# Performance work log

Measured on AMD Instinct MI355X. Metric: run time of the kernel, lower is better.

The kernel has to match this reference:

```python
import jax, jax.numpy as jnp
import numpy as np

LN_EPS = 1e-5


def setup_inputs() -> dict:
    key = jax.random.key(0)
    ks = jax.random.split(key, 6)
    N, E, D = 100000, 600000, 128
    x = jax.random.normal(ks[0], (N, D), dtype=jnp.float32)
    edge_index = jax.random.randint(ks[1], (2, E), 0, N, dtype=jnp.int64)
    dropout_mask = jax.random.uniform(ks[2], (N, D), dtype=jnp.float32)
    ln_gamma = jnp.ones((D,), dtype=jnp.float32)
    ln_beta = jnp.zeros((D,), dtype=jnp.float32)
    W_l = jax.random.normal(ks[3], (D, D), dtype=jnp.float32) / np.sqrt(D)
    b_l = jnp.zeros((D,), dtype=jnp.float32)
    W_r = jax.random.normal(ks[4], (D, D), dtype=jnp.float32) / np.sqrt(D)
    return {"x": x, "edge_index": edge_index, "dropout_mask": dropout_mask,
            "ln_gamma": ln_gamma, "ln_beta": ln_beta,
            "W_l": W_l, "b_l": b_l, "W_r": W_r}


def reference(x, edge_index, dropout_mask, ln_gamma, ln_beta, W_l, b_l, W_r):
    N = x.shape[0]
    # LayerNorm (elementwise affine) -> ReLU -> dropout mask
    mu = jnp.mean(x, axis=-1, keepdims=True)
    var = jnp.mean(jnp.square(x - mu), axis=-1, keepdims=True)
    h = (x - mu) * jax.lax.rsqrt(var + LN_EPS) * ln_gamma + ln_beta
    h = jax.nn.relu(h) * dropout_mask  # [N, D]
    # SAGEConv with mean aggregation: messages flow src -> dst
    src, dst = edge_index[0], edge_index[1]
    agg = jax.ops.segment_sum(h[src], dst, num_segments=N)  # [N, D]
    cnt = jax.ops.segment_sum(jnp.ones_like(dst, dtype=h.dtype), dst,
                              num_segments=N)
    mean_agg = agg / jnp.maximum(cnt, 1.0)[:, None]
    # out = lin_l(mean_agg) + lin_r(h); PyG stores weights as [out, in]
    return mean_agg @ W_l.T + b_l + h @ W_r.T
```

## Files before the change

kernel.cpp:

```cpp
#include <hip/hip_runtime.h>

#define LN_EPS 1e-5f
#define D 128
#define SCAN_CHUNK 1024
#define LDSA_STRIDE 264

typedef __attribute__((ext_vector_type(4))) float f32x4;
typedef __attribute__((ext_vector_type(8))) short bf16x8;

static __device__ __forceinline__ ushort f2bf(float f) {
    union { float f; unsigned u; } a; a.f = f;
    unsigned r = a.u + 0x7FFF + ((a.u >> 16) & 1);
    return (ushort)(r >> 16);
}
static __device__ __forceinline__ float bf2f(ushort u) {
    union { unsigned u; float f; } a; a.u = ((unsigned)u) << 16;
    return a.f;
}

__global__ void prep_w(const float* __restrict__ Wl,
                       const float* __restrict__ Wr,
                       ushort* __restrict__ Bfrag) {
    int t = blockIdx.x * blockDim.x + threadIdx.x;
    if (t >= 8 * 8 * 64 * 8) return;
    int i    = t & 7;
    int lane = (t >> 3) & 63;
    int jb   = (t >> 9) & 7;
    int ks   = t >> 12;
    int k = ks * 32 + (lane >> 4) * 8 + i;
    int j = jb * 16 + (lane & 15);
    float v = (k < D) ? Wl[j * D + k] : Wr[j * D + (k - D)];
    Bfrag[t] = f2bf(v);
}

__global__ void ln_hist(const float* __restrict__ x,
                        const float* __restrict__ mask,
                        const float* __restrict__ gamma,
                        const float* __restrict__ beta,
                        ushort* __restrict__ hbf,
                        const int* __restrict__ ei,
                        int* __restrict__ hist,
                        int N, int E, int lnBlocks) {
    if (blockIdx.x >= (unsigned)lnBlocks) {
        int e = (blockIdx.x - lnBlocks) * blockDim.x + threadIdx.x;
        if (e < E) atomicAdd(&hist[ei[E + e]], 1);
        return;
    }
    int node = (blockIdx.x * blockDim.x + threadIdx.x) >> 6;
    int lane = threadIdx.x & 63;
    if (node >= N) return;
    float2 v = ((const float2*)(x + (size_t)node * D))[lane];
    float s  = v.x + v.y;
    float ss = v.x * v.x + v.y * v.y;
#pragma unroll
    for (int off = 32; off > 0; off >>= 1) {
        s  += __shfl_xor(s, off);
        ss += __shfl_xor(ss, off);
    }
    float mu  = s * (1.0f / D);
    float var = ss * (1.0f / D) - mu * mu;
    float rs  = rsqrtf(var + LN_EPS);
    float2 g = ((const float2*)gamma)[lane];
    float2 b = ((const float2*)beta)[lane];
    float2 m = ((const float2*)(mask + (size_t)node * D))[lane];
    ushort2 o;
    o.x = f2bf(fmaxf((v.x - mu) * rs * g.x + b.x, 0.0f) * m.x);
    o.y = f2bf(fmaxf((v.y - mu) * rs * g.y + b.y, 0.0f) * m.y);
    ((ushort2*)(hbf + (size_t)node * D))[lane] = o;
}

__global__ void scan1(const int* __restrict__ hist, int* __restrict__ offs,
                      int* __restrict__ chunk_sums, int N) {
    __shared__ int lds[256];
    int base = blockIdx.x * SCAN_CHUNK;
    int t = threadIdx.x;
    int idx0 = base + t * 4;
    int v[4];
#pragma unroll
    for (int i = 0; i < 4; i++) {
        int idx = idx0 + i;
        v[i] = (idx < N) ? hist[idx] : 0;
    }
    lds[t] = v[0] + v[1] + v[2] + v[3];
    __syncthreads();
    for (int off = 1; off < 256; off <<= 1) {
        int add = (t >= off) ? lds[t - off] : 0;
        __syncthreads();
        lds[t] += add;
        __syncthreads();
    }
    int run = (t == 0) ? 0 : lds[t - 1];
    if (t == 255) chunk_sums[blockIdx.x] = lds[255];
#pragma unroll
    for (int i = 0; i < 4; i++) {
        int idx = idx0 + i;
        if (idx < N) offs[idx] = run;
        run += v[i];
    }
}

__global__ void scan_fix(int* __restrict__ offs, const int* __restrict__ csums,
                         int* __restrict__ cursor, int N) {
    __shared__ int base_s;
    int chunk = (blockIdx.x * 256) / SCAN_CHUNK;
    int t = threadIdx.x;
    if (t < 64) {
        int v = 0;
        for (int c = t; c < chunk; c += 64) v += csums[c];
#pragma unroll
        for (int off = 32; off > 0; off >>= 1) v += __shfl_xor(v, off);
        if (t == 0) base_s = v;
    }
    __syncthreads();
    int i = blockIdx.x * 256 + t;
    if (i >= N) return;
    int v = offs[i] + base_s;
    offs[i] = v;
    cursor[i] = v;
}

__global__ void sort_edges(const int* __restrict__ ei, int* __restrict__ cursor,
                           int* __restrict__ sorted_src, int E) {
    int e = blockIdx.x * blockDim.x + threadIdx.x;
    if (e >= E) return;
    int dst = ei[E + e];
    int pos = atomicAdd(&cursor[dst], 1);
    sorted_src[pos] = ei[e];
}

__global__ void aggregate4(const ushort* __restrict__ hbf,
                           const int* __restrict__ sorted_src,
                           const int* __restrict__ offs,
                           const int* __restrict__ hist,
                           ushort* __restrict__ magg, int N) {
    int wid  = (blockIdx.x * blockDim.x + threadIdx.x) >> 6;
    int lane = threadIdx.x & 63;
    int g  = lane >> 4;
    int sl = lane & 15;
    int node = wid * 4 + g;
    bool valid = node < N;
    int start = 0, deg = 0;
    if (valid) { start = offs[node]; deg = hist[node]; }
    float acc[8];
#pragma unroll
    for (int j = 0; j < 8; j++) acc[j] = 0.0f;
    int i = 0;
    for (; i + 2 <= deg; i += 2) {
        int s0 = sorted_src[start + i];
        int s1 = sorted_src[start + i + 1];
        bf16x8 v0 = *(const bf16x8*)(hbf + (size_t)s0 * D + sl * 8);
        bf16x8 v1 = *(const bf16x8*)(hbf + (size_t)s1 * D + sl * 8);
#pragma unroll
        for (int j = 0; j < 8; j++)
            acc[j] += bf2f((ushort)v0[j]) + bf2f((ushort)v1[j]);
    }
    if (i < deg) {
        int s0 = sorted_src[start + i];
        bf16x8 v0 = *(const bf16x8*)(hbf + (size_t)s0 * D + sl * 8);
#pragma unroll
        for (int j = 0; j < 8; j++) acc[j] += bf2f((ushort)v0[j]);
    }
    if (valid) {
        float inv = 1.0f / fmaxf((float)deg, 1.0f);
        bf16x8 o;
#pragma unroll
        for (int j = 0; j < 8; j++) o[j] = (short)f2bf(acc[j] * inv);
        *(bf16x8*)(magg + (size_t)node * D + sl * 8) = o;
    }
}

__global__ void __launch_bounds__(256, 3)
out_gemm_mfma(float* __restrict__ out,
              const ushort* __restrict__ magg,
              const ushort* __restrict__ hbf,
              const ushort* __restrict__ Bfrag,
              const float* __restrict__ bl,
              int N) {
    __shared__ ushort Alds[64 * LDSA_STRIDE];
    int tid  = threadIdx.x;
    int wave = tid >> 6;
    int lane = tid & 63;
    int n0 = blockIdx.x * 64;

    bf16x8 breg[8][2];
#pragma unroll
    for (int ks = 0; ks < 8; ks++)
#pragma unroll
        for (int jj = 0; jj < 2; jj++) {
            int jb = wave * 2 + jj;
            breg[ks][jj] = *(const bf16x8*)(Bfrag + (size_t)((ks * 8 + jb) * 64 + lane) * 8);
        }

#pragma unroll
    for (int it = 0; it < 4; it++) {
        int chunk = tid + 256 * it;
        int row = chunk >> 4;
        int c8  = chunk & 15;
        int node = n0 + row;
        bf16x8 va = (bf16x8){0,0,0,0,0,0,0,0};
        bf16x8 vh = (bf16x8){0,0,0,0,0,0,0,0};
        if (node < N) {
            va = *(const bf16x8*)(magg + (size_t)node * D + c8 * 8);
            vh = *(const bf16x8*)(hbf  + (size_t)node * D + c8 * 8);
        }
        *(bf16x8*)&Alds[row * LDSA_STRIDE + c8 * 8]       = va;
        *(bf16x8*)&Alds[row * LDSA_STRIDE + 128 + c8 * 8] = vh;
    }
    __syncthreads();

    f32x4 acc[4][2];
#pragma unroll
    for (int nb = 0; nb < 4; nb++)
#pragma unroll
        for (int jj = 0; jj < 2; jj++)
            acc[nb][jj] = (f32x4){0.f, 0.f, 0.f, 0.f};

    int arow = lane & 15;
    int akoff = (lane >> 4) * 8;
#pragma unroll
    for (int ks = 0; ks < 8; ks++) {
#pragma unroll
        for (int nb = 0; nb < 4; nb++) {
            bf16x8 a = *(const bf16x8*)&Alds[(nb * 16 + arow) * LDSA_STRIDE + ks * 32 + akoff];
            acc[nb][0] = __builtin_amdgcn_mfma_f32_16x16x32_bf16(a, breg[ks][0], acc[nb][0], 0, 0, 0);
            acc[nb][1] = __builtin_amdgcn_mfma_f32_16x16x32_bf16(a, breg[ks][1], acc[nb][1], 0, 0, 0);
        }
    }

    float bias0 = bl[wave * 32 + (lane & 15)];
    float bias1 = bl[wave * 32 + 16 + (lane & 15)];
    int rbase = (lane >> 4) * 4;
#pragma unroll
    for (int nb = 0; nb < 4; nb++) {
#pragma unroll
        for (int r = 0; r < 4; r++) {
            int row = nb * 16 + rbase + r;
            if (n0 + row < N) {
                float* orow = out + (size_t)(n0 + row) * D + wave * 32 + (lane & 15);
                orow[0]  = acc[nb][0][r] + bias0;
                orow[16] = acc[nb][1][r] + bias1;
            }
        }
    }
}

extern "C" void kernel_launch(void* const* d_in, const int* in_sizes, int n_in,
                              void* d_out, int out_size, void* d_ws, size_t ws_size,
                              hipStream_t stream) {
    const float* x     = (const float*)d_in[0];
    const int*   ei    = (const int*)  d_in[1];
    const float* mask  = (const float*)d_in[2];
    const float* gamma = (const float*)d_in[3];
    const float* beta  = (const float*)d_in[4];
    const float* Wl    = (const float*)d_in[5];
    const float* bl    = (const float*)d_in[6];
    const float* Wr    = (const float*)d_in[7];
    float* out = (float*)d_out;

    int N = in_sizes[0] / D;
    int E = in_sizes[1] / 2;
    int chunks = (N + SCAN_CHUNK - 1) / SCAN_CHUNK;

    ushort* hbf   = (ushort*)d_ws;
    ushort* magg  = hbf + (size_t)N * D;
    ushort* Bfrag = magg + (size_t)N * D;
    int* hist   = (int*)(Bfrag + 32768);
    int* offs   = hist + N;
    int* cursor = offs + N;
    int* csums  = cursor + N;
    int* ssrc   = csums + 128;

    int lnBlocks = (N + 3) / 4;
    int histBlocks = (E + 255) / 256;

    hipMemsetAsync(hist, 0, (size_t)N * sizeof(int), stream);
    prep_w<<<128, 256, 0, stream>>>(Wl, Wr, Bfrag);
    ln_hist<<<lnBlocks + histBlocks, 256, 0, stream>>>(x, mask, gamma, beta, hbf,
                                                       ei, hist, N, E, lnBlocks);
    scan1<<<chunks, 256, 0, stream>>>(hist, offs, csums, N);
    scan_fix<<<(N + 255) / 256, 256, 0, stream>>>(offs, csums, cursor, N);
    sort_edges<<<(E + 255) / 256, 256, 0, stream>>>(ei, cursor, ssrc, E);
    aggregate4<<<((N + 3) / 4 + 3) / 4, 256, 0, stream>>>(hbf, ssrc, offs, hist, magg, N);
    out_gemm_mfma<<<(N + 63) / 64, 256, 0, stream>>>(out, magg, hbf, Bfrag, bl, N);
}
```

Before: 263.7 us.

## Fuse neighbor aggregation into MFMA output GEMM and fold hist zeroing into prep

The mean aggregation now runs inside the GEMM kernel: each block gathers neighbor rows for its 64 nodes straight into LDS, so the intermediate magg buffer is no longer written to and read back from global memory, and one launch disappears. The hist memset is folded into prep_w. The LayerNorm kernel now handles two nodes per wave with float4 loads, and histogram blocks are placed first in the grid. In exchange, the GEMM kernel carries more registers and a divergent gather loop bounded by the largest degree among the four nodes each lane group handles.

```diff
diff --git a/kernel.cpp b/kernel.cpp
--- a/kernel.cpp
+++ b/kernel.cpp
@@ -20,17 +20,20 @@
 
 __global__ void prep_w(const float* __restrict__ Wl,
                        const float* __restrict__ Wr,
-                       ushort* __restrict__ Bfrag) {
+                       ushort* __restrict__ Bfrag,
+                       int* __restrict__ hist, int N) {
     int t = blockIdx.x * blockDim.x + threadIdx.x;
-    if (t >= 8 * 8 * 64 * 8) return;
-    int i    = t & 7;
-    int lane = (t >> 3) & 63;
-    int jb   = (t >> 9) & 7;
-    int ks   = t >> 12;
-    int k = ks * 32 + (lane >> 4) * 8 + i;
-    int j = jb * 16 + (lane & 15);
-    float v = (k < D) ? Wl[j * D + k] : Wr[j * D + (k - D)];
-    Bfrag[t] = f2bf(v);
+    if (t < 8 * 8 * 64 * 8) {
+        int i    = t & 7;
+        int lane = (t >> 3) & 63;
+        int jb   = (t >> 9) & 7;
+        int ks   = t >> 12;
+        int k = ks * 32 + (lane >> 4) * 8 + i;
+        int j = jb * 16 + (lane & 15);
+        float v = (k < D) ? Wl[j * D + k] : Wr[j * D + (k - D)];
+        Bfrag[t] = f2bf(v);
+    }
+    for (int i = t; i < N; i += gridDim.x * blockDim.x) hist[i] = 0;
 }
 
 __global__ void ln_hist(const float* __restrict__ x,
@@ -40,33 +43,37 @@
                         ushort* __restrict__ hbf,
                         const int* __restrict__ ei,
                         int* __restrict__ hist,
-                        int N, int E, int lnBlocks) {
-    if (blockIdx.x >= (unsigned)lnBlocks) {
-        int e = (blockIdx.x - lnBlocks) * blockDim.x + threadIdx.x;
+                        int N, int E, int histBlocks) {
+    if ((int)blockIdx.x < histBlocks) {
+        int e = blockIdx.x * blockDim.x + threadIdx.x;
         if (e < E) atomicAdd(&hist[ei[E + e]], 1);
         return;
     }
-    int node = (blockIdx.x * blockDim.x + threadIdx.x) >> 6;
     int lane = threadIdx.x & 63;
+    int wid  = (((int)blockIdx.x - histBlocks) * (int)blockDim.x + (int)threadIdx.x) >> 6;
+    int node = wid * 2 + (lane >> 5);
     if (node >= N) return;
-    float2 v = ((const float2*)(x + (size_t)node * D))[lane];
-    float s  = v.x + v.y;
-    float ss = v.x * v.x + v.y * v.y;
-#pragma unroll
-    for (int off = 32; off > 0; off >>= 1) {
+    int sl = lane & 31;
+    f32x4 v = ((const f32x4*)(x + (size_t)node * D))[sl];
+    float s  = v.x + v.y + v.z + v.w;
+    float ss = v.x * v.x + v.y * v.y + v.z * v.z + v.w * v.w;
+#pragma unroll
+    for (int off = 16; off > 0; off >>= 1) {
         s  += __shfl_xor(s, off);
         ss += __shfl_xor(ss, off);
     }
     float mu  = s * (1.0f / D);
     float var = ss * (1.0f / D) - mu * mu;
     float rs  = rsqrtf(var + LN_EPS);
-    float2 g = ((const float2*)gamma)[lane];
-    float2 b = ((const float2*)beta)[lane];
-    float2 m = ((const float2*)(mask + (size_t)node * D))[lane];
-    ushort2 o;
+    f32x4 g = ((const f32x4*)gamma)[sl];
+    f32x4 b = ((const f32x4*)beta)[sl];
+    f32x4 m = ((const f32x4*)(mask + (size_t)node * D))[sl];
+    ushort4 o;
     o.x = f2bf(fmaxf((v.x - mu) * rs * g.x + b.x, 0.0f) * m.x);
     o.y = f2bf(fmaxf((v.y - mu) * rs * g.y + b.y, 0.0f) * m.y);
-    ((ushort2*)(hbf + (size_t)node * D))[lane] = o;
+    o.z = f2bf(fmaxf((v.z - mu) * rs * g.z + b.z, 0.0f) * m.z);
+    o.w = f2bf(fmaxf((v.w - mu) * rs * g.w + b.w, 0.0f) * m.w);
+    ((ushort4*)(hbf + (size_t)node * D))[sl] = o;
 }
 
 __global__ void scan1(const int* __restrict__ hist, int* __restrict__ offs,
@@ -128,92 +135,84 @@
     sorted_src[pos] = ei[e];
 }
 
-__global__ void aggregate4(const ushort* __restrict__ hbf,
-                           const int* __restrict__ sorted_src,
-                           const int* __restrict__ offs,
-                           const int* __restrict__ hist,
-                           ushort* __restrict__ magg, int N) {
-    int wid  = (blockIdx.x * blockDim.x + threadIdx.x) >> 6;
-    int lane = threadIdx.x & 63;
-    int g  = lane >> 4;
-    int sl = lane & 15;
-    int node = wid * 4 + g;
-    bool valid = node < N;
-    int start = 0, deg = 0;
-    if (valid) { start = offs[node]; deg = hist[node]; }
-    float acc[8];
-#pragma unroll
-    for (int j = 0; j < 8; j++) acc[j] = 0.0f;
-    int i = 0;
-    for (; i + 2 <= deg; i += 2) {
-        int s0 = sorted_src[start + i];
-        int s1 = sorted_src[start + i + 1];
-        bf16x8 v0 = *(const bf16x8*)(hbf + (size_t)s0 * D + sl * 8);
-        bf16x8 v1 = *(const bf16x8*)(hbf + (size_t)s1 * D + sl * 8);
-#pragma unroll
-        for (int j = 0; j < 8; j++)
-            acc[j] += bf2f((ushort)v0[j]) + bf2f((ushort)v1[j]);
-    }
-    if (i < deg) {
-        int s0 = sorted_src[start + i];
-        bf16x8 v0 = *(const bf16x8*)(hbf + (size_t)s0 * D + sl * 8);
-#pragma unroll
-        for (int j = 0; j < 8; j++) acc[j] += bf2f((ushort)v0[j]);
-    }
-    if (valid) {
-        float inv = 1.0f / fmaxf((float)deg, 1.0f);
-        bf16x8 o;
-#pragma unroll
-        for (int j = 0; j < 8; j++) o[j] = (short)f2bf(acc[j] * inv);
-        *(bf16x8*)(magg + (size_t)node * D + sl * 8) = o;
-    }
-}
-
 __global__ void __launch_bounds__(256, 3)
-out_gemm_mfma(float* __restrict__ out,
-              const ushort* __restrict__ magg,
-              const ushort* __restrict__ hbf,
-              const ushort* __restrict__ Bfrag,
-              const float* __restrict__ bl,
-              int N) {
+agg_gemm(float* __restrict__ out,
+         const ushort* __restrict__ hbf,
+         const int* __restrict__ sorted_src,
+         const int* __restrict__ offs,
+         const int* __restrict__ hist,
+         const ushort* __restrict__ Bfrag,
+         const float* __restrict__ bl,
+         int N) {
     __shared__ ushort Alds[64 * LDSA_STRIDE];
     int tid  = threadIdx.x;
     int wave = tid >> 6;
     int lane = tid & 63;
     int n0 = blockIdx.x * 64;
 
-    bf16x8 breg[8][2];
-#pragma unroll
-    for (int ks = 0; ks < 8; ks++)
-#pragma unroll
-        for (int jj = 0; jj < 2; jj++) {
-            int jb = wave * 2 + jj;
-            breg[ks][jj] = *(const bf16x8*)(Bfrag + (size_t)((ks * 8 + jb) * 64 + lane) * 8);
-        }
-
 #pragma unroll
     for (int it = 0; it < 4; it++) {
         int chunk = tid + 256 * it;
         int row = chunk >> 4;
         int c8  = chunk & 15;
         int node = n0 + row;
-        bf16x8 va = (bf16x8){0,0,0,0,0,0,0,0};
         bf16x8 vh = (bf16x8){0,0,0,0,0,0,0,0};
-        if (node < N) {
-            va = *(const bf16x8*)(magg + (size_t)node * D + c8 * 8);
-            vh = *(const bf16x8*)(hbf  + (size_t)node * D + c8 * 8);
-        }
-        *(bf16x8*)&Alds[row * LDSA_STRIDE + c8 * 8]       = va;
+        if (node < N) vh = *(const bf16x8*)(hbf + (size_t)node * D + c8 * 8);
         *(bf16x8*)&Alds[row * LDSA_STRIDE + 128 + c8 * 8] = vh;
     }
+
+    int g  = lane >> 4;
+    int sl = lane & 15;
+    int row0 = wave * 16 + g;
+    int startp[4], degp[4];
+#pragma unroll
+    for (int p = 0; p < 4; p++) {
+        int node = n0 + row0 + p * 4;
+        startp[p] = 0; degp[p] = 0;
+        if (node < N) { startp[p] = offs[node]; degp[p] = hist[node]; }
+    }
+    float acc[4][8];
+#pragma unroll
+    for (int p = 0; p < 4; p++)
+#pragma unroll
+        for (int q = 0; q < 8; q++) acc[p][q] = 0.0f;
+    int dmax = max(max(degp[0], degp[1]), max(degp[2], degp[3]));
+    for (int j = 0; j < dmax; j++) {
+#pragma unroll
+        for (int p = 0; p < 4; p++) {
+            if (j < degp[p]) {
+                int s0 = sorted_src[startp[p] + j];
+                bf16x8 v = *(const bf16x8*)(hbf + (size_t)s0 * D + sl * 8);
+#pragma unroll
+                for (int q = 0; q < 8; q++) acc[p][q] += bf2f((ushort)v[q]);
+            }
+        }
+    }
+#pragma unroll
+    for (int p = 0; p < 4; p++) {
+        float inv = 1.0f / fmaxf((float)degp[p], 1.0f);
+        bf16x8 o;
+#pragma unroll
+        for (int q = 0; q < 8; q++) o[q] = (short)f2bf(acc[p][q] * inv);
+        *(bf16x8*)&Alds[(row0 + p * 4) * LDSA_STRIDE + sl * 8] = o;
+    }
     __syncthreads();
 
-    f32x4 acc[4][2];
+    bf16x8 breg[8][2];
+#pragma unroll
+    for (int ks = 0; ks < 8; ks++)
+#pragma unroll
+        for (int jj = 0; jj < 2; jj++) {
+            int jb = wave * 2 + jj;
+            breg[ks][jj] = *(const bf16x8*)(Bfrag + (size_t)((ks * 8 + jb) * 64 + lane) * 8);
+        }
+
+    f32x4 acc2[4][2];
 #pragma unroll
     for (int nb = 0; nb < 4; nb++)
 #pragma unroll
         for (int jj = 0; jj < 2; jj++)
-            acc[nb][jj] = (f32x4){0.f, 0.f, 0.f, 0.f};
+            acc2[nb][jj] = (f32x4){0.f, 0.f, 0.f, 0.f};
 
     int arow = lane & 15;
     int akoff = (lane >> 4) * 8;
@@ -222,8 +221,8 @@
 #pragma unroll
         for (int nb = 0; nb < 4; nb++) {
             bf16x8 a = *(const bf16x8*)&Alds[(nb * 16 + arow) * LDSA_STRIDE + ks * 32 + akoff];
-            acc[nb][0] = __builtin_amdgcn_mfma_f32_16x16x32_bf16(a, breg[ks][0], acc[nb][0], 0, 0, 0);
-            acc[nb][1] = __builtin_amdgcn_mfma_f32_16x16x32_bf16(a, breg[ks][1], acc[nb][1], 0, 0, 0);
+            acc2[nb][0] = __builtin_amdgcn_mfma_f32_16x16x32_bf16(a, breg[ks][0], acc2[nb][0], 0, 0, 0);
+            acc2[nb][1] = __builtin_amdgcn_mfma_f32_16x16x32_bf16(a, breg[ks][1], acc2[nb][1], 0, 0, 0);
         }
     }
 
@@ -237,8 +236,8 @@
             int row = nb * 16 + rbase + r;
             if (n0 + row < N) {
                 float* orow = out + (size_t)(n0 + row) * D + wave * 32 + (lane & 15);
-                orow[0]  = acc[nb][0][r] + bias0;
-                orow[16] = acc[nb][1][r] + bias1;
+                orow[0]  = acc2[nb][0][r] + bias0;
+                orow[16] = acc2[nb][1][r] + bias1;
             }
         }
     }
@@ -262,24 +261,21 @@
     int chunks = (N + SCAN_CHUNK - 1) / SCAN_CHUNK;
 
     ushort* hbf   = (ushort*)d_ws;
-    ushort* magg  = hbf + (size_t)N * D;
-    ushort* Bfrag = magg + (size_t)N * D;
+    ushort* Bfrag = hbf + (size_t)N * D;
     int* hist   = (int*)(Bfrag + 32768);
     int* offs   = hist + N;
     int* cursor = offs + N;
     int* csums  = cursor + N;
     int* ssrc   = csums + 128;
 
-    int lnBlocks = (N + 3) / 4;
     int histBlocks = (E + 255) / 256;
-
-    hipMemsetAsync(hist, 0, (size_t)N * sizeof(int), stream);
-    prep_w<<<128, 256, 0, stream>>>(Wl, Wr, Bfrag);
-    ln_hist<<<lnBlocks + histBlocks, 256, 0, stream>>>(x, mask, gamma, beta, hbf,
-                                                       ei, hist, N, E, lnBlocks);
+    int lnBlocks = (N + 7) / 8;
+
+    prep_w<<<512, 256, 0, stream>>>(Wl, Wr, Bfrag, hist, N);
+    ln_hist<<<histBlocks + lnBlocks, 256, 0, stream>>>(x, mask, gamma, beta, hbf,
+                                                       ei, hist, N, E, histBlocks);
     scan1<<<chunks, 256, 0, stream>>>(hist, offs, csums, N);
     scan_fix<<<(N + 255) / 256, 256, 0, stream>>>(offs, csums, cursor, N);
     sort_edges<<<(E + 255) / 256, 256, 0, stream>>>(ei, cursor, ssrc, E);
-    aggregate4<<<((N + 3) / 4 + 3) / 4, 256, 0, stream>>>(hbf, ssrc, offs, hist, magg, N);
-    out_gemm_mfma<<<(N + 63) / 64, 256, 0, stream>>>(out, magg, hbf, Bfrag, bl, N);
-}
+    agg_gemm<<<(N + 63) / 64, 256, 0, stream>>>(out, hbf, ssrc, offs, hist, Bfrag, bl, N);
+}
```

After: 286.6 us. 8.7% more time.
